# Performance work log

Measured on AMD Instinct MI355X. Metric: run time of the kernel, lower is better.

## Reference

```python
import jax, jax.numpy as jnp
import numpy as np

N = 10000          # num nodes
E = 160000         # num edges (avg degree 16)
F = 128            # num_features
S = 4              # num_species
RAD = 8            # radial_embedding_dim
RO = 16            # readout_mlp_irreps = 16x0e
EPS = 0.17677669529663687  # epsilon = 1/sqrt(avg_degree)
ACT_NORM = 1.679177        # normalize_function(silu): 1/sqrt(E[silu(x)^2]), x~N(0,1)


def nsilu(x):
    return jax.nn.silu(x) * ACT_NORM


def setup_inputs() -> dict:
    key = jax.random.key(0)
    ks = jax.random.split(key, 24)
    d = {}
    d["vectors"] = jax.random.normal(ks[0], (E, 3), jnp.float32)
    d["node_scalars"] = jax.random.normal(ks[1], (N, F), jnp.float32)
    d["node_vectors"] = jax.random.normal(ks[2], (N, F, 3), jnp.float32)
    d["radial_embeddings"] = jax.random.normal(ks[3], (E, RAD), jnp.float32)
    # linear_up (irrep-wise linear on 0e and 1o)
    d["W_up_s"] = jax.random.normal(ks[4], (F, F), jnp.float32)
    d["W_up_v"] = jax.random.normal(ks[5], (F, F), jnp.float32)
    # radial MLP [RAD,64,64,64,weight_dim=4F]
    d["W_mlp1"] = jax.random.normal(ks[6], (RAD, 64), jnp.float32) / np.sqrt(RAD)
    d["b_mlp1"] = jnp.zeros((64,), jnp.float32)
    d["W_mlp2"] = jax.random.normal(ks[7], (64, 64), jnp.float32) / np.sqrt(64.0)
    d["b_mlp2"] = jnp.zeros((64,), jnp.float32)
    d["W_mlp3"] = jax.random.normal(ks[8], (64, 64), jnp.float32) / np.sqrt(64.0)
    d["b_mlp3"] = jnp.zeros((64,), jnp.float32)
    d["W_mlp4"] = jax.random.normal(ks[9], (64, 4 * F), jnp.float32) / np.sqrt(64.0)
    d["b_mlp4"] = jnp.zeros((4 * F,), jnp.float32)
    # linear_down: TP out (2F x 0e + 2F x 1o) -> F x (0e+1o)
    d["W_down_s"] = jax.random.normal(ks[10], (2 * F, F), jnp.float32)
    d["W_down_v"] = jax.random.normal(ks[11], (2 * F, F), jnp.float32)
    # species-indexed skip linear (output is hidden_out = 0e only, since last=True)
    d["Wz_s"] = jax.random.normal(ks[12], (S, F, F), jnp.float32)
    # symmetric contraction weights: 5 invariant basis terms per channel per species
    d["W_sc"] = jax.random.normal(ks[13], (S, 5, F), jnp.float32)
    d["W_post"] = jax.random.normal(ks[14], (F, F), jnp.float32)
    d["W_ro1"] = jax.random.normal(ks[15], (F, RO), jnp.float32)
    d["W_ro2"] = jax.random.normal(ks[16], (RO, 1), jnp.float32)
    d["senders"] = jax.random.randint(ks[17], (E,), 0, N)
    d["receivers"] = jax.random.randint(ks[18], (E,), 0, N)
    d["num_species_counts"] = jnp.full((S,), N // S, dtype=jnp.int32)
    d["num_nodes"] = N
    return d


def reference(vectors, node_scalars, node_vectors, radial_embeddings,
              W_up_s, W_up_v,
              W_mlp1, b_mlp1, W_mlp2, b_mlp2, W_mlp3, b_mlp3, W_mlp4, b_mlp4,
              W_down_s, W_down_v, Wz_s, W_sc, W_post, W_ro1, W_ro2,
              senders, receivers, num_species_counts, num_nodes):
    # spherical harmonics (max_ell=1): Y0 = 1, Y1 = unit edge vector
    rnorm = jnp.linalg.norm(vectors, axis=-1, keepdims=True)
    Y1 = vectors / (rnorm + 1e-12)                      # [E,3]

    # species index per node from counts
    i = jnp.repeat(jnp.arange(S), num_species_counts, total_repeat_length=num_nodes)

    # self connection (species-indexed linear on input scalars; hidden_out = 0e)
    self_conn = jnp.einsum('nf,nfg->ng', node_scalars, Wz_s[i]) / np.sqrt(F)

    # linear_up (irrep-wise)
    s = node_scalars @ W_up_s / np.sqrt(F)              # [N,F]
    v = jnp.einsum('nfc,fg->ngc', node_vectors, W_up_v) / np.sqrt(F)  # [N,F,3]

    # radial MLP -> per-edge channelwise TP weights, 4 paths x F channels
    h = nsilu(radial_embeddings @ W_mlp1 + b_mlp1)
    h = nsilu(h @ W_mlp2 + b_mlp2)
    h = nsilu(h @ W_mlp3 + b_mlp3)
    mix = (h @ W_mlp4 + b_mlp4).reshape(-1, 4, F)       # [E,4,F]

    # channelwise tensor product: gather sender feats, combine with sph
    sg = s[senders]                                     # [E,F]
    vg = v[senders]                                     # [E,F,3]
    m_s0 = mix[:, 0] * sg                               # 0e x 0e -> 0e
    m_s3 = mix[:, 3] * (jnp.einsum('efc,ec->ef', vg, Y1) / np.sqrt(3.0))  # 1o x 1o -> 0e
    m_v1 = mix[:, 1][..., None] * sg[..., None] * Y1[:, None, :]          # 0e x 1o -> 1o
    m_v2 = mix[:, 2][..., None] * vg                                      # 1o x 0e -> 1o
    msg_s = jnp.concatenate([m_s0, m_s3], axis=-1)      # [E,2F]
    msg_v = jnp.concatenate([m_v1, m_v2], axis=1)       # [E,2F,3]

    # scatter to receivers
    agg_s = jax.ops.segment_sum(msg_s, receivers, num_segments=num_nodes) * EPS
    agg_v = jax.ops.segment_sum(msg_v, receivers, num_segments=num_nodes) * EPS

    # linear_down: 2F -> F per irrep
    s2 = agg_s @ W_down_s / np.sqrt(2 * F)              # [N,F]
    v2 = jnp.einsum('nfc,fg->ngc', agg_v, W_down_v) / np.sqrt(2 * F)  # [N,F,3]

    # symmetric contraction (correlation<=3, output 0e): per-species weighted
    # invariant basis {s, s^2, |v|^2, s^3, s|v|^2} per channel
    vv = jnp.sum(v2 * v2, axis=-1)                      # [N,F]
    basis = jnp.stack([s2, s2 * s2, vv, s2 * s2 * s2, s2 * vv], axis=1)  # [N,5,F]
    sc = jnp.sum(W_sc[i] * basis, axis=1)               # [N,F]

    feats = sc @ W_post / np.sqrt(F) + self_conn        # [N,F]

    # readout (last=True): linear -> scalar activation -> linear
    hr = nsilu(feats @ W_ro1 / np.sqrt(F))              # [N,16]
    node_outputs = hr @ W_ro2 / np.sqrt(RO)             # [N,1]
    return (node_outputs, feats)
```

## Files before the change

kernel.cpp:

```cpp
#include <hip/hip_runtime.h>
#include <hip/hip_bf16.h>
#include <math.h>

#define N_NODES 10000
#define N_EDGES 160000
#define F 128
#define TE 128
#define HS 72
#define JP2 516

typedef _Float16 v8h __attribute__((ext_vector_type(8)));
typedef _Float16 v4h __attribute__((ext_vector_type(4)));
typedef float    v4f __attribute__((ext_vector_type(4)));

__device__ __forceinline__ float nsilu(float x) {
    return 1.679177f * (x / (1.0f + expf(-x)));
}

__device__ __forceinline__ void fma4(float4& a, float s, const float4& b) {
    a.x = fmaf(s, b.x, a.x); a.y = fmaf(s, b.y, a.y);
    a.z = fmaf(s, b.z, a.z); a.w = fmaf(s, b.w, a.w);
}

__device__ __forceinline__ int species_of(int n, const int* __restrict__ counts) {
    int c0 = counts[0];
    int c01 = c0 + counts[1];
    int c012 = c01 + counts[2];
    return (n >= c0) + (n >= c01) + (n >= c012);
}

__global__ __launch_bounds__(256) void k_setup(
    const int* __restrict__ receivers, int* __restrict__ deg,
    const float* __restrict__ W2, const float* __restrict__ W3,
    const float* __restrict__ W4, const float* __restrict__ b4,
    const float* __restrict__ Wup_s, const float* __restrict__ Wup_v,
    const float* __restrict__ Wz, const float* __restrict__ Wds,
    const float* __restrict__ Wdv, const float* __restrict__ Wpost,
    _Float16* __restrict__ W2t, _Float16* __restrict__ W3t,
    _Float16* __restrict__ W4t, float* __restrict__ b4p,
    _Float16* __restrict__ Wup_s_t, _Float16* __restrict__ Wup_v_t,
    _Float16* __restrict__ Wz_t, _Float16* __restrict__ Wds_t,
    _Float16* __restrict__ Wdv_t, _Float16* __restrict__ Wpost_t,
    const float* __restrict__ ns, const float* __restrict__ nv,
    _Float16* __restrict__ ns16, _Float16* __restrict__ nv16)
{
    int gidx = blockIdx.x * 256 + threadIdx.x;
    if (gidx < N_EDGES) {
        atomicAdd(&deg[receivers[gidx]], 1);
        return;
    }
    int idx = gidx - N_EDGES;
    if (idx < 221696) {
        if (idx < 4096) {
            int u = idx >> 6, k = idx & 63;
            W2t[idx] = (_Float16)W2[k * 64 + u];
        } else if (idx < 8192) {
            int j = idx - 4096;
            int u = j >> 6, k = j & 63;
            W3t[j] = (_Float16)W3[k * 64 + u];
        } else if (idx < 40960) {
            int j = idx - 8192;
            int gn = j >> 6, k = j & 63;
            int go = (gn & 3) * 128 + (gn >> 2);
            W4t[j] = (_Float16)W4[k * 512 + go];
        } else if (idx < 41472) {
            int j = idx - 40960;
            int go = (j & 3) * 128 + (j >> 2);
            b4p[j] = b4[go];
        } else if (idx < 57856) {
            int j = idx - 41472;
            int g = j >> 7, f = j & 127;
            Wup_s_t[j] = (_Float16)Wup_s[f * 128 + g];
        } else if (idx < 74240) {
            int j = idx - 57856;
            int g = j >> 7, f = j & 127;
            Wup_v_t[j] = (_Float16)Wup_v[f * 128 + g];
        } else if (idx < 139776) {
            int j = idx - 74240;
            int s = j >> 14, r = j & 16383;
            int g = r >> 7, f = r & 127;
            Wz_t[j] = (_Float16)Wz[s * 16384 + f * 128 + g];
        } else if (idx < 172544) {
            int j = idx - 139776;
            int g = j >> 8, k = j & 255;
            Wds_t[j] = (_Float16)Wds[k * 128 + g];
        } else if (idx < 205312) {
            int j = idx - 172544;
            int g = j >> 8, k = j & 255;
            Wdv_t[j] = (_Float16)Wdv[k * 128 + g];
        } else {
            int j = idx - 205312;
            int g = j >> 7, f = j & 127;
            Wpost_t[j] = (_Float16)Wpost[f * 128 + g];
        }
        return;
    }
    int j = idx - 221696;
    if (j < N_NODES * F) {
        ns16[j] = (_Float16)ns[j];
    } else if (j < 4 * N_NODES * F) {
        int j2 = j - N_NODES * F;
        int row = j2 >> 7, f = j2 & 127;
        int n = row / 3, c = row - n * 3;
        nv16[j2] = (_Float16)nv[((size_t)n * F + f) * 3 + c];
    }
}

__global__ __launch_bounds__(1024) void k_scan(const int* __restrict__ deg,
                                               int* __restrict__ offs,
                                               int* __restrict__ cursor) {
    __shared__ int sums[1024];
    const int t = threadIdx.x;
    const int CH = 10;
    int base = t * CH;
    int local[CH];
    int s = 0;
    #pragma unroll
    for (int j = 0; j < CH; ++j) {
        int v = (base + j < N_NODES) ? deg[base + j] : 0;
        local[j] = s;
        s += v;
    }
    sums[t] = s;
    __syncthreads();
    for (int off = 1; off < 1024; off <<= 1) {
        int v = (t >= off) ? sums[t - off] : 0;
        __syncthreads();
        sums[t] += v;
        __syncthreads();
    }
    int carry = (t == 0) ? 0 : sums[t - 1];
    #pragma unroll
    for (int j = 0; j < CH; ++j) {
        int idx = base + j;
        if (idx < N_NODES) {
            int o = carry + local[j];
            offs[idx] = o;
            cursor[idx] = o;
        }
    }
    if (t == 1023) offs[N_NODES] = sums[1023];
}

__global__ __launch_bounds__(256) void k_fill(const int* __restrict__ receivers,
                                              const int* __restrict__ senders,
                                              const float* __restrict__ vectors,
                                              int* __restrict__ cursor,
                                              int* __restrict__ pcsr,
                                              float4* __restrict__ yq) {
    int e = blockIdx.x * 256 + threadIdx.x;
    if (e < N_EDGES) {
        int pos = atomicAdd(&cursor[receivers[e]], 1);
        pcsr[e] = pos;
        float vx = vectors[e * 3 + 0];
        float vy = vectors[e * 3 + 1];
        float vz = vectors[e * 3 + 2];
        float inv = 1.0f / (sqrtf(vx * vx + vy * vy + vz * vz) + 1e-12f);
        float4 y;
        y.x = vx * inv; y.y = vy * inv; y.z = vz * inv;
        y.w = __int_as_float(senders[e]);
        yq[pos] = y;
    }
}

template <int K>
__device__ __forceinline__ void gemm_tile(
    const _Float16* __restrict__ A, const _Float16* __restrict__ Bg,
    float* __restrict__ out, int M, int row0, float scale,
    _Float16* Bl, const int* __restrict__ counts, int sp)
{
    const int t = threadIdx.x;
    constexpr int KP = K + 8;
    __syncthreads();
    for (int idx = t; idx < 128 * (K / 8); idx += 256) {
        int g = idx / (K / 8), kk = (idx % (K / 8)) * 8;
        *(v8h*)(Bl + g * KP + kk) = *(const v8h*)(Bg + g * K + kk);
    }
    __syncthreads();

    const int lane = t & 63;
    const int w = t >> 6;
    const int c = lane & 15;
    const int q = lane >> 4;

    v4f acc[2][8];
    #pragma unroll
    for (int mi = 0; mi < 2; ++mi)
        #pragma unroll
        for (int nt = 0; nt < 8; ++nt)
            acc[mi][nt] = (v4f){0.f, 0.f, 0.f, 0.f};

    for (int ch = 0; ch < K / 32; ++ch) {
        v8h a[2];
        #pragma unroll
        for (int mi = 0; mi < 2; ++mi) {
            int r = row0 + (2 * w + mi) * 16 + c;
            r = min(r, M - 1);
            a[mi] = *(const v8h*)(A + (size_t)r * K + ch * 32 + q * 8);
        }
        #pragma unroll
        for (int nt = 0; nt < 8; ++nt) {
            v8h b = *(const v8h*)(Bl + (nt * 16 + c) * KP + ch * 32 + q * 8);
            acc[0][nt] = __builtin_amdgcn_mfma_f32_16x16x32_f16(a[0], b, acc[0][nt], 0, 0, 0);
            acc[1][nt] = __builtin_amdgcn_mfma_f32_16x16x32_f16(a[1], b, acc[1][nt], 0, 0, 0);
        }
    }
    #pragma unroll
    for (int mi = 0; mi < 2; ++mi) {
        #pragma unroll
        for (int r = 0; r < 4; ++r) {
            int row = row0 + (2 * w + mi) * 16 + q * 4 + r;
            bool ok = row < M;
            if (ok && sp >= 0) ok = (species_of(row, counts) == sp);
            if (ok) {
                float* op = out + (size_t)row * 128;
                #pragma unroll
                for (int nt = 0; nt < 8; ++nt)
                    op[nt * 16 + c] = acc[mi][nt][r] * scale;
            }
        }
    }
}

__global__ __launch_bounds__(256) void k_gemm_up(
    const _Float16* __restrict__ ns16, const _Float16* __restrict__ nv16,
    const _Float16* __restrict__ Wup_s_t, const _Float16* __restrict__ Wup_v_t,
    const _Float16* __restrict__ Wz_t, const int* __restrict__ counts,
    float* __restrict__ s_buf, float* __restrict__ v_buf, float* __restrict__ selfc)
{
    __shared__ _Float16 Bl[128 * 136];
    const int row0 = blockIdx.x * 128;
    const float isf = 0.08838834764831845f;
    if (blockIdx.y == 0) {
        if (row0 >= N_NODES) return;
        gemm_tile<128>(ns16, Wup_s_t, s_buf, N_NODES, row0, isf, Bl, counts, -1);
    } else if (blockIdx.y == 1) {
        gemm_tile<128>(nv16, Wup_v_t, v_buf, 3 * N_NODES, row0, isf, Bl, counts, -1);
    } else {
        if (row0 >= N_NODES) return;
        int sp0 = species_of(row0, counts);
        int sp1 = species_of(min(row0 + 127, N_NODES - 1), counts);
        for (int sp = sp0; sp <= sp1; ++sp)
            gemm_tile<128>(ns16, Wz_t + (size_t)sp * 16384, selfc,
                           N_NODES, row0, isf, Bl, counts, sp);
    }
}

__global__ __launch_bounds__(256) void k_gemm_down(
    const _Float16* __restrict__ agg_s16, const _Float16* __restrict__ agg_v16,
    const _Float16* __restrict__ Wds_t, const _Float16* __restrict__ Wdv_t,
    const int* __restrict__ counts,
    float* __restrict__ s2, float* __restrict__ v2)
{
    __shared__ _Float16 Bl[128 * 264];
    const int row0 = blockIdx.x * 128;
    if (blockIdx.y == 0) {
        if (row0 >= N_NODES) return;
        gemm_tile<256>(agg_s16, Wds_t, s2, N_NODES, row0, 1.0f, Bl, counts, -1);
    } else {
        gemm_tile<256>(agg_v16, Wdv_t, v2, 3 * N_NODES, row0, 1.0f, Bl, counts, -1);
    }
}

__device__ __forceinline__ void mfma_layer64(
    const _Float16* src, _Float16* dst,
    const _Float16* __restrict__ Wt, const float* __restrict__ b,
    int w, int q, int c)
{
    v8h B[4][2];
    float bias[4];
    #pragma unroll
    for (int nt = 0; nt < 4; ++nt) {
        B[nt][0] = *(const v8h*)(Wt + (nt * 16 + c) * 64 + q * 8);
        B[nt][1] = *(const v8h*)(Wt + (nt * 16 + c) * 64 + 32 + q * 8);
        bias[nt] = b[nt * 16 + c];
    }
    #pragma unroll
    for (int mi = 0; mi < 2; ++mi) {
        int mt = 2 * w + mi;
        v8h a0 = *(const v8h*)(src + (mt * 16 + c) * HS + q * 8);
        v8h a1 = *(const v8h*)(src + (mt * 16 + c) * HS + 32 + q * 8);
        #pragma unroll
        for (int nt = 0; nt < 4; ++nt) {
            v4f acc = {bias[nt], bias[nt], bias[nt], bias[nt]};
            acc = __builtin_amdgcn_mfma_f32_16x16x32_f16(a0, B[nt][0], acc, 0, 0, 0);
            acc = __builtin_amdgcn_mfma_f32_16x16x32_f16(a1, B[nt][1], acc, 0, 0, 0);
            #pragma unroll
            for (int r = 0; r < 4; ++r)
                dst[(mt * 16 + q * 4 + r) * HS + nt * 16 + c] = (_Float16)nsilu(acc[r]);
        }
    }
}

__global__ __launch_bounds__(256) void k_mlp(
    const float* __restrict__ re,
    const float* __restrict__ W1, const float* __restrict__ b1,
    const _Float16* __restrict__ W2t, const float* __restrict__ b2,
    const _Float16* __restrict__ W3t, const float* __restrict__ b3,
    const _Float16* __restrict__ W4t, const float* __restrict__ b4p,
    const int* __restrict__ pcsr,
    _Float16* __restrict__ mix)
{
    __shared__ float sre[TE * 8];
    __shared__ _Float16 hA[TE * HS];
    __shared__ _Float16 hB[TE * HS];
    __shared__ int spos[TE];

    const int t = threadIdx.x;
    const int e0 = blockIdx.x * TE;

    ((float4*)sre)[t] = ((const float4*)(re + (size_t)e0 * 8))[t];
    if (t < TE) spos[t] = pcsr[e0 + t];
    __syncthreads();

    {
        const int uslot = t & 15;
        const int egrp = t >> 4;
        const int u0 = uslot * 4;
        float4 w[8];
        #pragma unroll
        for (int k = 0; k < 8; ++k) w[k] = *(const float4*)(W1 + k * 64 + u0);
        float4 bb = *(const float4*)(b1 + u0);
        #pragma unroll
        for (int i = 0; i < 8; ++i) {
            int e = egrp + i * 16;
            const float* rp = sre + e * 8;
            float4 a = bb;
            #pragma unroll
            for (int k = 0; k < 8; ++k) fma4(a, rp[k], w[k]);
            v4h r = {(_Float16)nsilu(a.x), (_Float16)nsilu(a.y),
                     (_Float16)nsilu(a.z), (_Float16)nsilu(a.w)};
            *(v4h*)(hA + e * HS + u0) = r;
        }
    }
    __syncthreads();

    const int lane = t & 63;
    const int w = t >> 6;
    const int c = lane & 15;
    const int q = lane >> 4;

    mfma_layer64(hA, hB, W2t, b2, w, q, c);
    mfma_layer64(hB, hA, W3t, b3, w, q, c);
    __syncthreads();

    v8h B4[8][2];
    float bias4[8];
    #pragma unroll
    for (int j = 0; j < 8; ++j) {
        int g = (8 * w + j) * 16 + c;
        B4[j][0] = *(const v8h*)(W4t + g * 64 + q * 8);
        B4[j][1] = *(const v8h*)(W4t + g * 64 + 32 + q * 8);
        bias4[j] = b4p[g];
    }
    _Float16* stage = hB;
    for (int mt = 0; mt < 8; ++mt) {
        v8h a0 = *(const v8h*)(hA + (mt * 16 + c) * HS + q * 8);
        v8h a1 = *(const v8h*)(hA + (mt * 16 + c) * HS + 32 + q * 8);
        #pragma unroll
        for (int j = 0; j < 8; ++j) {
            v4f acc = {bias4[j], bias4[j], bias4[j], bias4[j]};
            acc = __builtin_amdgcn_mfma_f32_16x16x32_f16(a0, B4[j][0], acc, 0, 0, 0);
            acc = __builtin_amdgcn_mfma_f32_16x16x32_f16(a1, B4[j][1], acc, 0, 0, 0);
            int col = (8 * w + j) * 16 + c;
            #pragma unroll
            for (int r = 0; r < 4; ++r)
                stage[(q * 4 + r) * JP2 + col] = (_Float16)acc[r];
        }
        __syncthreads();
        {
            int row = t & 15, seg = t >> 4;
            int pg = spos[mt * 16 + row];
            const _Float16* sp = stage + row * JP2 + seg * 32;
            _Float16* dp = mix + (size_t)pg * 512 + seg * 32;
            #pragma unroll
            for (int k = 0; k < 8; ++k)
                *(v4h*)(dp + k * 4) = *(const v4h*)(sp + k * 4);
        }
        __syncthreads();
    }
}

__global__ __launch_bounds__(128) void k_gather(
    const _Float16* __restrict__ mix, const float4* __restrict__ yq,
    const float* __restrict__ s_buf, const float* __restrict__ v_buf,
    const int* __restrict__ offs,
    _Float16* __restrict__ agg_s16, _Float16* __restrict__ agg_v16)
{
    const int n = blockIdx.x;
    const int f = threadIdx.x;
    const int beg = offs[n], end = offs[n + 1];
    const float inv_sqrt3 = 0.5773502691896258f;

    float as0 = 0, as1 = 0;
    float av00 = 0, av01 = 0, av02 = 0, av10 = 0, av11 = 0, av12 = 0;

    for (int p = beg; p < end; ++p) {
        float4 y = yq[p];
        int snd = __float_as_int(y.w);

        union { uint2 u; _Float16 h[4]; } mu;
        mu.u = *(const uint2*)(mix + (size_t)p * 512 + f * 4);
        float m0 = (float)mu.h[0];
        float m1 = (float)mu.h[1];
        float m2 = (float)mu.h[2];
        float m3 = (float)mu.h[3];

        float sg = s_buf[(size_t)snd * F + f];
        const float* vb = v_buf + (size_t)snd * 384;
        float vg0 = vb[f];
        float vg1 = vb[128 + f];
        float vg2 = vb[256 + f];

        as0 += m0 * sg;
        as1 += m3 * (vg0 * y.x + vg1 * y.y + vg2 * y.z) * inv_sqrt3;
        float w1s = m1 * sg;
        av00 += w1s * y.x; av01 += w1s * y.y; av02 += w1s * y.z;
        av10 += m2 * vg0;  av11 += m2 * vg1;  av12 += m2 * vg2;
    }
    const float SC = 0.011048543456039804f;
    agg_s16[(size_t)n * 256 + f]       = (_Float16)(as0 * SC);
    agg_s16[(size_t)n * 256 + 128 + f] = (_Float16)(as1 * SC);
    _Float16* av = agg_v16 + (size_t)n * 768;
    av[0 * 256 + f]       = (_Float16)(av00 * SC);
    av[0 * 256 + 128 + f] = (_Float16)(av10 * SC);
    av[1 * 256 + f]       = (_Float16)(av01 * SC);
    av[1 * 256 + 128 + f] = (_Float16)(av11 * SC);
    av[2 * 256 + f]       = (_Float16)(av02 * SC);
    av[2 * 256 + 128 + f] = (_Float16)(av12 * SC);
}

__global__ __launch_bounds__(256) void k_contract(
    const float* __restrict__ s2, const float* __restrict__ v2,
    const float* __restrict__ Wsc, const int* __restrict__ counts,
    _Float16* __restrict__ sc16)
{
    int idx = blockIdx.x * 256 + threadIdx.x;
    int n = idx >> 7, g = idx & 127;
    float s = s2[idx];
    const float* vp = v2 + (size_t)n * 384;
    float a0 = vp[g], a1 = vp[128 + g], a2 = vp[256 + g];
    float vv = a0 * a0 + a1 * a1 + a2 * a2;
    const float* w = Wsc + (size_t)species_of(n, counts) * 640;
    float sc = w[g] * s + w[128 + g] * (s * s) + w[256 + g] * vv
             + w[384 + g] * (s * s * s) + w[512 + g] * (s * vv);
    sc16[idx] = (_Float16)sc;
}

__global__ __launch_bounds__(256) void k_post(
    const _Float16* __restrict__ sc16, const _Float16* __restrict__ Wpost_t,
    const float* __restrict__ selfc,
    const float* __restrict__ Wro1, const float* __restrict__ Wro2,
    float* __restrict__ out)
{
    __shared__ _Float16 Bl[128 * 136];
    __shared__ float sfeat[128][132];
    __shared__ float shr[128][16];
    const int t = threadIdx.x;
    const int row0 = blockIdx.x * 128;
    const float isf = 0.08838834764831845f;

    for (int idx = t; idx < 128 * 16; idx += 256) {
        int g = idx >> 4, kk = (idx & 15) * 8;
        *(v8h*)(Bl + g * 136 + kk) = *(const v8h*)(Wpost_t + g * 128 + kk);
    }
    __syncthreads();

    const int lane = t & 63;
    const int w = t >> 6;
    const int c = lane & 15;
    const int q = lane >> 4;

    v4f acc[2][8];
    #pragma unroll
    for (int mi = 0; mi < 2; ++mi)
        #pragma unroll
        for (int nt = 0; nt < 8; ++nt)
            acc[mi][nt] = (v4f){0.f, 0.f, 0.f, 0.f};

    for (int ch = 0; ch < 4; ++ch) {
        v8h a[2];
        #pragma unroll
        for (int mi = 0; mi < 2; ++mi) {
            int r = row0 + (2 * w + mi) * 16 + c;
            r = min(r, N_NODES - 1);
            a[mi] = *(const v8h*)(sc16 + (size_t)r * 128 + ch * 32 + q * 8);
        }
        #pragma unroll
        for (int nt = 0; nt < 8; ++nt) {
            v8h b = *(const v8h*)(Bl + (nt * 16 + c) * 136 + ch * 32 + q * 8);
            acc[0][nt] = __builtin_amdgcn_mfma_f32_16x16x32_f16(a[0], b, acc[0][nt], 0, 0, 0);
            acc[1][nt] = __builtin_amdgcn_mfma_f32_16x16x32_f16(a[1], b, acc[1][nt], 0, 0, 0);
        }
    }
    #pragma unroll
    for (int mi = 0; mi < 2; ++mi) {
        #pragma unroll
        for (int r = 0; r < 4; ++r) {
            int row = row0 + (2 * w + mi) * 16 + q * 4 + r;
            int rl = (2 * w + mi) * 16 + q * 4 + r;
            if (row < N_NODES) {
                #pragma unroll
                for (int nt = 0; nt < 8; ++nt) {
                    int col = nt * 16 + c;
                    float feat = acc[mi][nt][r] * isf + selfc[(size_t)row * 128 + col];
                    out[N_NODES + (size_t)row * 128 + col] = feat;
                    sfeat[rl][col] = feat;
                }
            } else {
                #pragma unroll
                for (int nt = 0; nt < 8; ++nt) sfeat[rl][nt * 16 + c] = 0.f;
            }
        }
    }
    __syncthreads();

    for (int idx = t; idx < 2048; idx += 256) {
        int nd = idx >> 4, u = idx & 15;
        float a = 0;
        for (int f = 0; f < 128; f += 4) {
            float4 x = *(const float4*)&sfeat[nd][f];
            a += x.x * Wro1[(f + 0) * 16 + u] + x.y * Wro1[(f + 1) * 16 + u]
               + x.z * Wro1[(f + 2) * 16 + u] + x.w * Wro1[(f + 3) * 16 + u];
        }
        shr[nd][u] = nsilu(a * isf);
    }
    __syncthreads();

    if (t < 128 && row0 + t < N_NODES) {
        float a = 0;
        #pragma unroll
        for (int j = 0; j < 16; ++j) a += shr[t][j] * Wro2[j];
        out[row0 + t] = a * 0.25f;
    }
}


extern "C" void kernel_launch(void* const* d_in, const int* in_sizes, int n_in,
                              void* d_out, int out_size, void* d_ws, size_t ws_size,
                              hipStream_t stream) {
    const float* vectors      = (const float*)d_in[0];
    const float* node_scalars = (const float*)d_in[1];
    const float* node_vectors = (const float*)d_in[2];
    const float* radial       = (const float*)d_in[3];
    const float* W_up_s       = (const float*)d_in[4];
    const float* W_up_v       = (const float*)d_in[5];
    const float* W1 = (const float*)d_in[6];
    const float* b1 = (const float*)d_in[7];
    const float* W2 = (const float*)d_in[8];
    const float* b2 = (const float*)d_in[9];
    const float* W3 = (const float*)d_in[10];
    const float* b3 = (const float*)d_in[11];
    const float* W4 = (const float*)d_in[12];
    const float* b4 = (const float*)d_in[13];
    const float* Wds  = (const float*)d_in[14];
    const float* Wdv  = (const float*)d_in[15];
    const float* Wz   = (const float*)d_in[16];
    const float* Wsc  = (const float*)d_in[17];
    const float* Wpost= (const float*)d_in[18];
    const float* Wro1 = (const float*)d_in[19];
    const float* Wro2 = (const float*)d_in[20];
    const int* senders   = (const int*)d_in[21];
    const int* receivers = (const int*)d_in[22];
    const int* counts    = (const int*)d_in[23];
    float* out = (float*)d_out;

    const size_t NF = (size_t)N_NODES * F;

    char* base = (char*)d_ws;
    _Float16* mix = (_Float16*)base;
    float* s2   = (float*)base;
    float* v2   = s2 + NF;
    _Float16* sc16 = (_Float16*)(v2 + 3 * NF);

    char* p = base + (size_t)N_EDGES * 512 * 2;
    float4* yq     = (float4*)p;          p += (size_t)N_EDGES * 16;
    _Float16* ns16 = (_Float16*)p;        p += NF * 2;
    _Float16* nv16 = (_Float16*)p;        p += 3 * NF * 2;
    float* s_buf   = (float*)p;           p += NF * 4;
    float* v_buf   = (float*)p;           p += 3 * NF * 4;
    float* selfc   = (float*)p;           p += NF * 4;
    _Float16* agg_s16 = (_Float16*)p;     p += 2 * NF * 2;
    _Float16* agg_v16 = (_Float16*)p;     p += 6 * NF * 2;
    int* pcsr   = (int*)p;                p += (size_t)N_EDGES * 4;
    int* deg    = (int*)p;                p += N_NODES * 4;
    int* offs   = (int*)p;                p += (N_NODES + 1) * 4 + 12;
    int* cursor = (int*)p;                p += N_NODES * 4;
    _Float16* W2t = (_Float16*)p;         p += 4096 * 2;
    _Float16* W3t = (_Float16*)p;         p += 4096 * 2;
    _Float16* W4t = (_Float16*)p;         p += 32768 * 2;
    float* b4p    = (float*)p;            p += 512 * 4;
    _Float16* Wup_s_t = (_Float16*)p;     p += 16384 * 2;
    _Float16* Wup_v_t = (_Float16*)p;     p += 16384 * 2;
    _Float16* Wz_t    = (_Float16*)p;     p += 65536 * 2;
    _Float16* Wds_t   = (_Float16*)p;     p += 32768 * 2;
    _Float16* Wdv_t   = (_Float16*)p;     p += 32768 * 2;
    _Float16* Wpost_t = (_Float16*)p;     p += 16384 * 2;

    hipMemsetAsync(deg, 0, N_NODES * sizeof(int), stream);

    k_setup<<<21491, 256, 0, stream>>>(
        receivers, deg, W2, W3, W4, b4, W_up_s, W_up_v, Wz, Wds, Wdv, Wpost,
        W2t, W3t, W4t, b4p, Wup_s_t, Wup_v_t, Wz_t, Wds_t, Wdv_t, Wpost_t,
        node_scalars, node_vectors, ns16, nv16);

    k_scan<<<1, 1024, 0, stream>>>(deg, offs, cursor);

    k_fill<<<(N_EDGES + 255) / 256, 256, 0, stream>>>(
        receivers, senders, vectors, cursor, pcsr, yq);

    k_gemm_up<<<dim3(235, 3), 256, 0, stream>>>(
        ns16, nv16, Wup_s_t, Wup_v_t, Wz_t, counts, s_buf, v_buf, selfc);

    k_mlp<<<N_EDGES / TE, 256, 0, stream>>>(
        radial, W1, b1, W2t, b2, W3t, b3, W4t, b4p, pcsr, mix);

    k_gather<<<N_NODES, 128, 0, stream>>>(
        mix, yq, s_buf, v_buf, offs, agg_s16, agg_v16);

    k_gemm_down<<<dim3(235, 2), 256, 0, stream>>>(
        agg_s16, agg_v16, Wds_t, Wdv_t, counts, s2, v2);

    k_contract<<<(N_NODES * F) / 256, 256, 0, stream>>>(s2, v2, Wsc, counts, sc16);

    k_post<<<(N_NODES + 127) / 128, 256, 0, stream>>>(
        sc16, Wpost_t, selfc, Wro1, Wro2, out);
}
```

Before: 354.8 us.

## Permute radial embeddings into CSR order so MLP writes mix rows directly

k_fill now scatters each edge's radial embedding into receiver-sorted (CSR) position, so k_mlp processes edges already in CSR order. Each block can then write its output rows straight to global memory at contiguous positions, without staging through LDS and two barriers per row tile. The CSR radial buffer reuses the agg_v16 workspace, which is free until k_gather runs. The gather loop also gains an unroll pragma. The risk is that the direct global stores are 2-byte scattered writes per lane instead of the earlier vectorized v4h stores.

New measurement: 328.1 us. 7.5% less time.

```diff
diff --git a/kernel.cpp b/kernel.cpp
--- a/kernel.cpp
+++ b/kernel.cpp
@@ -7,7 +7,6 @@
 #define F 128
 #define TE 128
 #define HS 72
-#define JP2 516
 
 typedef _Float16 v8h __attribute__((ext_vector_type(8)));
 typedef _Float16 v4h __attribute__((ext_vector_type(4)));
@@ -145,13 +144,13 @@
 __global__ __launch_bounds__(256) void k_fill(const int* __restrict__ receivers,
                                               const int* __restrict__ senders,
                                               const float* __restrict__ vectors,
+                                              const float* __restrict__ radial,
                                               int* __restrict__ cursor,
-                                              int* __restrict__ pcsr,
-                                              float4* __restrict__ yq) {
+                                              float4* __restrict__ yq,
+                                              float4* __restrict__ re_csr) {
     int e = blockIdx.x * 256 + threadIdx.x;
     if (e < N_EDGES) {
         int pos = atomicAdd(&cursor[receivers[e]], 1);
-        pcsr[e] = pos;
         float vx = vectors[e * 3 + 0];
         float vy = vectors[e * 3 + 1];
         float vz = vectors[e * 3 + 2];
@@ -160,6 +159,9 @@
         y.x = vx * inv; y.y = vy * inv; y.z = vz * inv;
         y.w = __int_as_float(senders[e]);
         yq[pos] = y;
+        const float4* rp = (const float4*)(radial + (size_t)e * 8);
+        re_csr[pos * 2]     = rp[0];
+        re_csr[pos * 2 + 1] = rp[1];
     }
 }
 
@@ -293,24 +295,21 @@
 }
 
 __global__ __launch_bounds__(256) void k_mlp(
-    const float* __restrict__ re,
+    const float* __restrict__ re_csr,
     const float* __restrict__ W1, const float* __restrict__ b1,
     const _Float16* __restrict__ W2t, const float* __restrict__ b2,
     const _Float16* __restrict__ W3t, const float* __restrict__ b3,
     const _Float16* __restrict__ W4t, const float* __restrict__ b4p,
-    const int* __restrict__ pcsr,
     _Float16* __restrict__ mix)
 {
     __shared__ float sre[TE * 8];
     __shared__ _Float16 hA[TE * HS];
     __shared__ _Float16 hB[TE * HS];
-    __shared__ int spos[TE];
 
     const int t = threadIdx.x;
-    const int e0 = blockIdx.x * TE;
-
-    ((float4*)sre)[t] = ((const float4*)(re + (size_t)e0 * 8))[t];
-    if (t < TE) spos[t] = pcsr[e0 + t];
+    const int p0 = blockIdx.x * TE;
+
+    ((float4*)sre)[t] = ((const float4*)(re_csr + (size_t)p0 * 8))[t];
     __syncthreads();
 
     {
@@ -353,31 +352,20 @@
         B4[j][1] = *(const v8h*)(W4t + g * 64 + 32 + q * 8);
         bias4[j] = b4p[g];
     }
-    _Float16* stage = hB;
     for (int mt = 0; mt < 8; ++mt) {
         v8h a0 = *(const v8h*)(hA + (mt * 16 + c) * HS + q * 8);
         v8h a1 = *(const v8h*)(hA + (mt * 16 + c) * HS + 32 + q * 8);
+        size_t rowbase = (size_t)(p0 + mt * 16 + q * 4) * 512;
         #pragma unroll
         for (int j = 0; j < 8; ++j) {
             v4f acc = {bias4[j], bias4[j], bias4[j], bias4[j]};
             acc = __builtin_amdgcn_mfma_f32_16x16x32_f16(a0, B4[j][0], acc, 0, 0, 0);
             acc = __builtin_amdgcn_mfma_f32_16x16x32_f16(a1, B4[j][1], acc, 0, 0, 0);
-            int col = (8 * w + j) * 16 + c;
+            int gcol = (8 * w + j) * 16 + c;
             #pragma unroll
             for (int r = 0; r < 4; ++r)
-                stage[(q * 4 + r) * JP2 + col] = (_Float16)acc[r];
-        }
-        __syncthreads();
-        {
-            int row = t & 15, seg = t >> 4;
-            int pg = spos[mt * 16 + row];
-            const _Float16* sp = stage + row * JP2 + seg * 32;
-            _Float16* dp = mix + (size_t)pg * 512 + seg * 32;
-            #pragma unroll
-            for (int k = 0; k < 8; ++k)
-                *(v4h*)(dp + k * 4) = *(const v4h*)(sp + k * 4);
-        }
-        __syncthreads();
+                mix[rowbase + (size_t)r * 512 + gcol] = (_Float16)acc[r];
+        }
     }
 }
 
@@ -395,6 +383,7 @@
     float as0 = 0, as1 = 0;
     float av00 = 0, av01 = 0, av02 = 0, av10 = 0, av11 = 0, av12 = 0;
 
+    #pragma unroll 4
     for (int p = beg; p < end; ++p) {
         float4 y = yq[p];
         int snd = __float_as_int(y.w);
@@ -582,7 +571,6 @@
     float* selfc   = (float*)p;           p += NF * 4;
     _Float16* agg_s16 = (_Float16*)p;     p += 2 * NF * 2;
     _Float16* agg_v16 = (_Float16*)p;     p += 6 * NF * 2;
-    int* pcsr   = (int*)p;                p += (size_t)N_EDGES * 4;
     int* deg    = (int*)p;                p += N_NODES * 4;
     int* offs   = (int*)p;                p += (N_NODES + 1) * 4 + 12;
     int* cursor = (int*)p;                p += N_NODES * 4;
@@ -597,6 +585,8 @@
     _Float16* Wdv_t   = (_Float16*)p;     p += 32768 * 2;
     _Float16* Wpost_t = (_Float16*)p;     p += 16384 * 2;
 
+    float4* re_csr = (float4*)agg_v16;
+
     hipMemsetAsync(deg, 0, N_NODES * sizeof(int), stream);
 
     k_setup<<<21491, 256, 0, stream>>>(
@@ -607,13 +597,13 @@
     k_scan<<<1, 1024, 0, stream>>>(deg, offs, cursor);
 
     k_fill<<<(N_EDGES + 255) / 256, 256, 0, stream>>>(
-        receivers, senders, vectors, cursor, pcsr, yq);
+        receivers, senders, vectors, radial, cursor, yq, re_csr);
 
     k_gemm_up<<<dim3(235, 3), 256, 0, stream>>>(
         ns16, nv16, Wup_s_t, Wup_v_t, Wz_t, counts, s_buf, v_buf, selfc);
 
     k_mlp<<<N_EDGES / TE, 256, 0, stream>>>(
-        radial, W1, b1, W2t, b2, W3t, b3, W4t, b4p, pcsr, mix);
+        (const float*)re_csr, W1, b1, W2t, b2, W3t, b3, W4t, b4p, mix);
 
     k_gather<<<N_NODES, 128, 0, stream>>>(
         mix, yq, s_buf, v_buf, offs, agg_s16, agg_v16);
```
